# Kernel optimization log

Hardware: AMD Instinct MI355X
Metric: run time of the kernel (lower is better)

## Reference

```python
import jax, jax.numpy as jnp
import numpy as np

VOLRADIUS = 64.0
DT = 1.0 / VOLRADIUS          # normalized step size (dt / volradius)
NSTEPS = 64                   # covers t in [0, 1.0) at step DT


def setup_inputs() -> dict:
    key = jax.random.key(0)
    ks = jax.random.split(key, 8)
    B, H, W, K, M = 1, 128, 128, 32, 16
    # ray origins near volume center, unit directions
    raypos = 0.2 * jax.random.normal(ks[0], (B, H, W, 3), jnp.float32)
    rd = jax.random.normal(ks[1], (B, H, W, 3), jnp.float32)
    raydir = rd / jnp.linalg.norm(rd, axis=-1, keepdims=True)
    tmin = jnp.zeros((B, H, W), jnp.float32)
    tmax = 0.9 + 0.1 * jax.random.uniform(ks[2], (B, H, W), dtype=jnp.float32)
    tminmax = jnp.stack([tmin, tmax], axis=-1)
    # primitive poses: positions, rotations (orthonormal via QR), inverse-scales
    primpos = 0.3 * jax.random.normal(ks[3], (B, K, 3), jnp.float32)
    A = jax.random.normal(ks[4], (B, K, 3, 3), jnp.float32)
    primrot, _ = jnp.linalg.qr(A)
    primscale = 1.0 + 2.0 * jax.random.uniform(ks[5], (B, K, 3), dtype=jnp.float32)
    # RGBA voxel payload per primitive; alpha channel nonnegative (decoder emits nonneg density)
    template = jax.random.normal(ks[6], (B, K, 4, M, M, M), jnp.float32)
    template = template.at[:, :, 3].set(2.0 * jax.nn.softplus(template[:, :, 3]))
    return dict(raypos=raypos, raydir=raydir, tminmax=tminmax, primpos=primpos,
                primrot=primrot, primscale=primscale, template=template)


def _trilinear(template, y):
    # template [B,K,C,M,M,M]; y [B,R,K,3] normalized coords in [-1,1] (align_corners)
    B, K, C, M = template.shape[0], template.shape[1], template.shape[2], template.shape[3]
    g = (y + 1.0) * 0.5 * (M - 1)
    i0 = jnp.clip(jnp.floor(g), 0, M - 2).astype(jnp.int32)
    f = jnp.clip(g - i0.astype(g.dtype), 0.0, 1.0)
    i1 = i0 + 1
    bidx = jnp.arange(B)[:, None, None]
    kidx = jnp.arange(K)[None, None, :]

    def corner(iz, iy, ix):
        # advanced-index gather -> [B,R,K,C]
        return template[bidx, kidx, :, iz, iy, ix]

    fz, fy, fx = f[..., 0:1], f[..., 1:2], f[..., 2:3]
    i0z, i0y, i0x = i0[..., 0], i0[..., 1], i0[..., 2]
    i1z, i1y, i1x = i1[..., 0], i1[..., 1], i1[..., 2]
    v = ((1 - fz) * (1 - fy) * (1 - fx) * corner(i0z, i0y, i0x)
         + (1 - fz) * (1 - fy) * fx * corner(i0z, i0y, i1x)
         + (1 - fz) * fy * (1 - fx) * corner(i0z, i1y, i0x)
         + (1 - fz) * fy * fx * corner(i0z, i1y, i1x)
         + fz * (1 - fy) * (1 - fx) * corner(i1z, i0y, i0x)
         + fz * (1 - fy) * fx * corner(i1z, i0y, i1x)
         + fz * fy * (1 - fx) * corner(i1z, i1y, i0x)
         + fz * fy * fx * corner(i1z, i1y, i1x))
    return v  # [B,R,K,C]


def reference(raypos, raydir, tminmax, primpos, primrot, primscale, template):
    B, H, W, _ = raypos.shape
    R = H * W
    rp = raypos.reshape(B, R, 3)
    rd = raydir.reshape(B, R, 3)
    tmm = tminmax.reshape(B, R, 2)
    tmin, tmax = tmm[..., 0:1], tmm[..., 1:2]

    def step(carry, i):
        rgb, alpha = carry
        t = tmin + i * DT                                   # [B,R,1]
        pos = rp + rd * t                                   # [B,R,3]
        xl = pos[:, :, None, :] - primpos[:, None, :, :]    # [B,R,K,3]
        yloc = jnp.einsum('bkij,brkj->brki', primrot, xl) * primscale[:, None, :, :]
        inside = jnp.all(jnp.abs(yloc) <= 1.0, axis=-1, keepdims=True).astype(rgb.dtype)
        samp = (_trilinear(template, yloc) * inside).sum(axis=2)   # [B,R,4]
        srgb, salpha = samp[..., :3], samp[..., 3:4]
        valid = (t < tmax).astype(rgb.dtype)
        # clamped additive compositing (Neural Volumes / MVP)
        newalpha = jnp.clip(alpha + salpha * DT * valid, 0.0, 1.0)
        contrib = newalpha - alpha
        return (rgb + srgb * contrib, newalpha), None

    init = (jnp.zeros((B, R, 3), raypos.dtype), jnp.zeros((B, R, 1), raypos.dtype))
    (rgb, alpha), _ = jax.lax.scan(step, init, jnp.arange(NSTEPS, dtype=raypos.dtype))

    rayrgba = jnp.concatenate([rgb, alpha], axis=-1).reshape(B, H, W, 4)
    rayrgba = jnp.transpose(rayrgba, (0, 3, 1, 2))   # [B,4,H,W]
    rayrgb = rayrgba[:, :3]
    rayalpha = rayrgba[:, 3:4]
    return rayrgb, rayalpha, rayrgba
```

## Files before the change

### kernel.cpp

```cpp
#include <hip/hip_runtime.h>
#include <hip/hip_fp16.h>


namespace {

constexpr float kDT  = 1.0f / 64.0f;
constexpr int   kVox = 32 * 4096;

struct H4 { __half2 lo, hi; };
struct __attribute__((aligned(8))) H4x2 { __half2 l0, h0, l1, h1; };

__global__ __launch_bounds__(256) void transpose_tmpl_h(
    const float* __restrict__ tmpl, H4* __restrict__ wsH)
{
    const int idx = blockIdx.x * 256 + threadIdx.x;
    const int k   = idx >> 12;
    const int rem = idx & 4095;
    const float* src = tmpl + k * 16384 + rem;
    H4 v;
    v.lo = __floats2half2_rn(src[0],    src[4096]);
    v.hi = __floats2half2_rn(src[8192], src[12288]);
    wsH[idx] = v;
}

__device__ __forceinline__ __half2 lerp2(__half2 a, __half2 b, __half2 f) {
    return __hfma2(f, __hsub2(b, a), a);
}

template<int CTRL>
__device__ __forceinline__ float dpp_add(float v) {
    return v + __int_as_float(__builtin_amdgcn_update_dpp(
        0, __float_as_int(v), CTRL, 0xF, 0xF, true));
}

__device__ __forceinline__ float half_sum32(float v) {
    v = dpp_add<0xB1>(v);
    v = dpp_add<0x4E>(v);
    v = dpp_add<0x141>(v);
    v = dpp_add<0x140>(v);
    v += __int_as_float(__builtin_amdgcn_ds_swizzle(__float_as_int(v), 0x401F));
    return v;
}

__global__ __launch_bounds__(256) void raymarch12(
    const float* __restrict__ raypos,
    const float* __restrict__ raydir,
    const float* __restrict__ tminmax,
    const float* __restrict__ primpos,
    const float* __restrict__ primrot,
    const float* __restrict__ primscale,
    const H4* __restrict__ wsH,
    float* __restrict__ out,
    int R)
{
    const int lane   = threadIdx.x & 63;
    const int wid    = threadIdx.x >> 6;
    const int k      = lane & 31;
    const int parity = lane >> 5;
    const int ray    = blockIdx.x * 4 + wid;

    const float rpx = raypos[ray * 3 + 0];
    const float rpy = raypos[ray * 3 + 1];
    const float rpz = raypos[ray * 3 + 2];
    const float rdx = raydir[ray * 3 + 0];
    const float rdy = raydir[ray * 3 + 1];
    const float rdz = raydir[ray * 3 + 2];
    const float tmin = tminmax[ray * 2 + 0];
    const float tmax = tminmax[ray * 2 + 1];

    float A0, A1, A2, D0, D1, D2;
    {
        const float ox = rpx - primpos[k * 3 + 0];
        const float oy = rpy - primpos[k * 3 + 1];
        const float oz = rpz - primpos[k * 3 + 2];
        const float s0 = primscale[k * 3 + 0];
        const float s1 = primscale[k * 3 + 1];
        const float s2 = primscale[k * 3 + 2];
        const float* rk = primrot + k * 9;
        A0 = (rk[0] * ox + rk[1] * oy + rk[2] * oz) * s0;
        D0 = (rk[0] * rdx + rk[1] * rdy + rk[2] * rdz) * s0;
        A1 = (rk[3] * ox + rk[4] * oy + rk[5] * oz) * s1;
        D1 = (rk[3] * rdx + rk[4] * rdy + rk[5] * rdz) * s1;
        A2 = (rk[6] * ox + rk[7] * oy + rk[8] * oz) * s2;
        D2 = (rk[6] * rdx + rk[7] * rdy + rk[8] * rdz) * s2;
    }

    const H4* __restrict__ tbase = wsH + k * 4096;

    float alpha = 0.f;
    float r0 = 0.f, r1 = 0.f, r2 = 0.f;

    bool  inA, inB;
    int   adA, adB;
    float fzA, fyA, fxA, fzB, fyB, fxB;
    H4x2  a00, a01, a10, a11, b00, b01, b10, b11;

#define COORDS(J, IN, AD, FZ, FY, FX)                                    \
    {                                                                    \
        const float tl = fmaf((float)(2 * (J) + parity), kDT, tmin);     \
        const float y0 = fmaf(D0, tl, A0);                               \
        const float y1 = fmaf(D1, tl, A1);                               \
        const float y2 = fmaf(D2, tl, A2);                               \
        IN = ((J) < 32) && (tl < tmax) && fabsf(y0) <= 1.0f              \
           && fabsf(y1) <= 1.0f && fabsf(y2) <= 1.0f;                    \
        const float gz = fmaf(y0, 7.5f, 7.5f);                           \
        const float gy = fmaf(y1, 7.5f, 7.5f);                           \
        const float gx = fmaf(y2, 7.5f, 7.5f);                           \
        const int iz = min((int)gz, 14);                                 \
        const int iy = min((int)gy, 14);                                 \
        const int ix = min((int)gx, 14);                                 \
        FZ = fminf(gz - (float)iz, 1.0f);                                \
        FY = fminf(gy - (float)iy, 1.0f);                                \
        FX = fminf(gx - (float)ix, 1.0f);                                \
        AD = iz * 256 + iy * 16 + ix;                                    \
    }

#define PREF(IN, AD, P00, P01, P10, P11)                                 \
    if (IN) {                                                            \
        const H4* tp = tbase + (AD);                                     \
        P00 = *(const H4x2*)(tp + 0);                                    \
        P01 = *(const H4x2*)(tp + 16);                                   \
        P10 = *(const H4x2*)(tp + 256);                                  \
        P11 = *(const H4x2*)(tp + 272);                                  \
    }

#define CONSUME(J, IN, FZ, FY, FX, P00, P01, P10, P11)                   \
    {                                                                    \
        float s0 = 0.f, s1 = 0.f, s2 = 0.f, s3 = 0.f;                    \
        if (IN) {                                                        \
            const __half2 hz = __float2half2_rn(FZ);                     \
            const __half2 hy = __float2half2_rn(FY);                     \
            const __half2 hx = __float2half2_rn(FX);                     \
            const __half2 q0l0 = lerp2(P00.l0, P10.l0, hz);              \
            const __half2 q0h0 = lerp2(P00.h0, P10.h0, hz);              \
            const __half2 q0l1 = lerp2(P00.l1, P10.l1, hz);              \
            const __half2 q0h1 = lerp2(P00.h1, P10.h1, hz);              \
            const __half2 q1l0 = lerp2(P01.l0, P11.l0, hz);              \
            const __half2 q1h0 = lerp2(P01.h0, P11.h0, hz);              \
            const __half2 q1l1 = lerp2(P01.l1, P11.l1, hz);              \
            const __half2 q1h1 = lerp2(P01.h1, P11.h1, hz);              \
            const __half2 ul0 = lerp2(q0l0, q1l0, hy);                   \
            const __half2 uh0 = lerp2(q0h0, q1h0, hy);                   \
            const __half2 ul1 = lerp2(q0l1, q1l1, hy);                   \
            const __half2 uh1 = lerp2(q0h1, q1h1, hy);                   \
            const __half2 vl = lerp2(ul0, ul1, hx);                      \
            const __half2 vh = lerp2(uh0, uh1, hx);                      \
            const float2 fLo = __half22float2(vl);                       \
            const float2 fHi = __half22float2(vh);                       \
            s0 = fLo.x; s1 = fLo.y; s2 = fHi.x; s3 = fHi.y;              \
        }                                                                \
        if (__ballot(IN)) {                                              \
            float tot = half_sum32(s3);                                  \
            const float other = __shfl_xor(tot, 32);                     \
            const float te = parity ? other : tot;       \
            const float to = parity ? tot : other;       \
              \
            const float na1 = fminf(fmaf(te, kDT, alpha), 1.0f);         \
            const float c_e = na1 - alpha;                               \
            const float na2 = fminf(fmaf(to, kDT, na1), 1.0f);           \
            const float c_o = na2 - na1;                                 \
            alpha = na2;                                                 \
            const float contrib = parity ? c_o : c_e;                    \
            r0 = fmaf(s0, contrib, r0);                                  \
            r1 = fmaf(s1, contrib, r1);                                  \
            r2 = fmaf(s2, contrib, r2);                                  \
        }                                                                \
    }

    COORDS(0, inA, adA, fzA, fyA, fxA);
    PREF(inA, adA, a00, a01, a10, a11);

    for (int j = 0; ; ) {
        COORDS(j + 1, inB, adB, fzB, fyB, fxB);
        PREF(inB, adB, b00, b01, b10, b11);
        CONSUME(j, inA, fzA, fyA, fxA, a00, a01, a10, a11);
        ++j;
        {
            const float t0 = fmaf((float)(2 * j), kDT, tmin);
            if (j >= 32 || t0 >= tmax || alpha >= 1.0f) break;
        }
        COORDS(j + 1, inA, adA, fzA, fyA, fxA);
        PREF(inA, adA, a00, a01, a10, a11);
        CONSUME(j, inB, fzB, fyB, fxB, b00, b01, b10, b11);
        ++j;
        {
            const float t0 = fmaf((float)(2 * j), kDT, tmin);
            if (j >= 32 || t0 >= tmax || alpha >= 1.0f) break;
        }
    }

#undef COORDS
#undef PREF
#undef CONSUME

    r0 = half_sum32(r0); r0 += __shfl_xor(r0, 32);
    r1 = half_sum32(r1); r1 += __shfl_xor(r1, 32);
    r2 = half_sum32(r2); r2 += __shfl_xor(r2, 32);

    if (lane == 0) {
        out[0 * R + ray] = r0;
        out[1 * R + ray] = r1;
        out[2 * R + ray] = r2;
        out[3 * R + ray] = alpha;
        out[4 * R + ray] = r0;
        out[5 * R + ray] = r1;
        out[6 * R + ray] = r2;
        out[7 * R + ray] = alpha;
    }
}

__global__ __launch_bounds__(256) void raymarch_fb(
    const float* __restrict__ raypos, const float* __restrict__ raydir,
    const float* __restrict__ tminmax, const float* __restrict__ primpos,
    const float* __restrict__ primrot, const float* __restrict__ primscale,
    const float* __restrict__ tmpl, float* __restrict__ out, int R)
{
    const int lane = threadIdx.x & 63;
    const int wid  = threadIdx.x >> 6;
    const int k    = lane & 31;
    const int half = lane >> 5;
    const int ray  = blockIdx.x * 8 + wid * 2 + half;

    const float rpx = raypos[ray*3+0], rpy = raypos[ray*3+1], rpz = raypos[ray*3+2];
    const float rdx = raydir[ray*3+0], rdy = raydir[ray*3+1], rdz = raydir[ray*3+2];
    const float tmin = tminmax[ray*2+0], tmax = tminmax[ray*2+1];

    float A0,A1,A2,D0,D1,D2;
    {
        const float ox = rpx - primpos[k*3+0], oy = rpy - primpos[k*3+1], oz = rpz - primpos[k*3+2];
        const float s0 = primscale[k*3+0], s1 = primscale[k*3+1], s2 = primscale[k*3+2];
        const float* rk = primrot + k*9;
        A0 = (rk[0]*ox+rk[1]*oy+rk[2]*oz)*s0; D0 = (rk[0]*rdx+rk[1]*rdy+rk[2]*rdz)*s0;
        A1 = (rk[3]*ox+rk[4]*oy+rk[5]*oz)*s1; D1 = (rk[3]*rdx+rk[4]*rdy+rk[5]*rdz)*s1;
        A2 = (rk[6]*ox+rk[7]*oy+rk[8]*oz)*s2; D2 = (rk[6]*rdx+rk[7]*rdy+rk[8]*rdz)*s2;
    }
    float alpha = 0.f, r0 = 0.f, r1 = 0.f, r2 = 0.f;
    for (int i = 0; i < 64; ++i) {
        const float t = fmaf((float)i, kDT, tmin);
        const bool live = (t < tmax) && (alpha < 1.0f);
        if (__ballot(live) == 0ull) break;
        const float y0 = fmaf(D0,t,A0), y1 = fmaf(D1,t,A1), y2 = fmaf(D2,t,A2);
        const bool inside = live && fabsf(y0)<=1.f && fabsf(y1)<=1.f && fabsf(y2)<=1.f;
        if (__ballot(inside) == 0ull) continue;
        float s0=0.f,s1=0.f,s2=0.f,s3=0.f;
        if (inside) {
            const float gz=(y0+1.f)*7.5f, gy=(y1+1.f)*7.5f, gx=(y2+1.f)*7.5f;
            const int iz=(int)fminf(floorf(gz),14.f), iy=(int)fminf(floorf(gy),14.f), ix=(int)fminf(floorf(gx),14.f);
            const float fz=fminf(gz-(float)iz,1.f), fy=fminf(gy-(float)iy,1.f), fx=fminf(gx-(float)ix,1.f);
            const float oz_=1.f-fz, oy_=1.f-fy, ox_=1.f-fx;
            const float w000=oz_*oy_*ox_, w001=oz_*oy_*fx, w010=oz_*fy*ox_, w011=oz_*fy*fx;
            const float w100=fz*oy_*ox_, w101=fz*oy_*fx, w110=fz*fy*ox_, w111=fz*fy*fx;
            const float* tp = tmpl + k*16384 + iz*256 + iy*16 + ix;
            float acc[4];
            #pragma unroll
            for (int c = 0; c < 4; ++c) {
                const float* tc = tp + c*4096;
                acc[c] = w000*tc[0]+w001*tc[1]+w010*tc[16]+w011*tc[17]
                       + w100*tc[256]+w101*tc[257]+w110*tc[272]+w111*tc[273];
            }
            s0=acc[0]; s1=acc[1]; s2=acc[2]; s3=acc[3];
        }
        float tot3 = s3;
        #pragma unroll
        for (int m = 1; m < 32; m <<= 1) tot3 += __shfl_xor(tot3, m);
        const float na = fminf(fmaf(tot3, kDT, alpha), 1.0f);
        const float contrib = na - alpha;
        alpha = na;
        r0 = fmaf(s0, contrib, r0); r1 = fmaf(s1, contrib, r1); r2 = fmaf(s2, contrib, r2);
    }
    #pragma unroll
    for (int m = 1; m < 32; m <<= 1) {
        r0 += __shfl_xor(r0, m); r1 += __shfl_xor(r1, m); r2 += __shfl_xor(r2, m);
    }
    if (k == 0) {
        out[0*R+ray]=r0; out[1*R+ray]=r1; out[2*R+ray]=r2; out[3*R+ray]=alpha;
        out[4*R+ray]=r0; out[5*R+ray]=r1; out[6*R+ray]=r2; out[7*R+ray]=alpha;
    }
}

}

extern "C" void kernel_launch(void* const* d_in, const int* in_sizes, int n_in,
                              void* d_out, int out_size, void* d_ws, size_t ws_size,
                              hipStream_t stream) {
    const float* raypos    = (const float*)d_in[0];
    const float* raydir    = (const float*)d_in[1];
    const float* tminmax   = (const float*)d_in[2];
    const float* primpos   = (const float*)d_in[3];
    const float* primrot   = (const float*)d_in[4];
    const float* primscale = (const float*)d_in[5];
    const float* tmpl      = (const float*)d_in[6];
    float* out = (float*)d_out;

    const int R = in_sizes[0] / 3;
    const size_t needH = (size_t)kVox * sizeof(H4);

    if (ws_size >= needH) {
        H4* wsH = (H4*)d_ws;
        transpose_tmpl_h<<<dim3(kVox / 256), dim3(256), 0, stream>>>(tmpl, wsH);
        raymarch12<<<dim3(R / 4), dim3(256), 0, stream>>>(
            raypos, raydir, tminmax, primpos, primrot, primscale, wsH, out, R);
    } else {
        raymarch_fb<<<dim3(R / 8), dim3(256), 0, stream>>>(
            raypos, raydir, tminmax, primpos, primrot, primscale, tmpl, out, R);
    }
}
```

Baseline: 90.35 us.

## Process four steps per iteration instead of software-prefetched two-step pipeline

The explicit A/B prefetch double-buffering loop is replaced by a loop that handles four samples per iteration (two per lane parity), issuing both sets of gathers together and then running the compositing chain for all four. The aim is to halve loop and early-exit check overhead and the number of reductions per iteration, while still keeping two gathers in flight. The trade-off is that gathers are no longer issued an iteration ahead, so latency hiding depends on the compiler and on occupancy. Early termination is also coarser, so a ray may do up to one extra pair of samples after saturating.

```diff
diff --git a/kernel.cpp b/kernel.cpp
--- a/kernel.cpp
+++ b/kernel.cpp
@@ -42,7 +42,7 @@
     return v;
 }
 
-__global__ __launch_bounds__(256) void raymarch12(
+__global__ __launch_bounds__(256) void raymarch13(
     const float* __restrict__ raypos,
     const float* __restrict__ raydir,
     const float* __restrict__ tminmax,
@@ -90,18 +90,13 @@
     float alpha = 0.f;
     float r0 = 0.f, r1 = 0.f, r2 = 0.f;
 
-    bool  inA, inB;
-    int   adA, adB;
-    float fzA, fyA, fxA, fzB, fyB, fxB;
-    H4x2  a00, a01, a10, a11, b00, b01, b10, b11;
-
-#define COORDS(J, IN, AD, FZ, FY, FX)                                    \
+#define COORDS(SUB, IN, AD, FZ, FY, FX)                                  \
     {                                                                    \
-        const float tl = fmaf((float)(2 * (J) + parity), kDT, tmin);     \
+        const float tl = fmaf((float)(SUB), kDT, tmin);                  \
         const float y0 = fmaf(D0, tl, A0);                               \
         const float y1 = fmaf(D1, tl, A1);                               \
         const float y2 = fmaf(D2, tl, A2);                               \
-        IN = ((J) < 32) && (tl < tmax) && fabsf(y0) <= 1.0f              \
+        IN = (tl < tmax) && fabsf(y0) <= 1.0f                            \
            && fabsf(y1) <= 1.0f && fabsf(y2) <= 1.0f;                    \
         const float gz = fmaf(y0, 7.5f, 7.5f);                           \
         const float gy = fmaf(y1, 7.5f, 7.5f);                           \
@@ -115,30 +110,26 @@
         AD = iz * 256 + iy * 16 + ix;                                    \
     }
 
-#define PREF(IN, AD, P00, P01, P10, P11)                                 \
-    if (IN) {                                                            \
-        const H4* tp = tbase + (AD);                                     \
-        P00 = *(const H4x2*)(tp + 0);                                    \
-        P01 = *(const H4x2*)(tp + 16);                                   \
-        P10 = *(const H4x2*)(tp + 256);                                  \
-        P11 = *(const H4x2*)(tp + 272);                                  \
-    }
-
-#define CONSUME(J, IN, FZ, FY, FX, P00, P01, P10, P11)                   \
+#define EVAL(IN, AD, FZ, FY, FX, S0, S1, S2, S3)                         \
     {                                                                    \
-        float s0 = 0.f, s1 = 0.f, s2 = 0.f, s3 = 0.f;                    \
+        S0 = 0.f; S1 = 0.f; S2 = 0.f; S3 = 0.f;                         \
         if (IN) {                                                        \
+            const H4* tp = tbase + (AD);                                 \
+            const H4x2 p00 = *(const H4x2*)(tp + 0);                     \
+            const H4x2 p01 = *(const H4x2*)(tp + 16);                    \
+            const H4x2 p10 = *(const H4x2*)(tp + 256);                   \
+            const H4x2 p11 = *(const H4x2*)(tp + 272);                   \
             const __half2 hz = __float2half2_rn(FZ);                     \
             const __half2 hy = __float2half2_rn(FY);                     \
             const __half2 hx = __float2half2_rn(FX);                     \
-            const __half2 q0l0 = lerp2(P00.l0, P10.l0, hz);              \
-            const __half2 q0h0 = lerp2(P00.h0, P10.h0, hz);              \
-            const __half2 q0l1 = lerp2(P00.l1, P10.l1, hz);              \
-            const __half2 q0h1 = lerp2(P00.h1, P10.h1, hz);              \
-            const __half2 q1l0 = lerp2(P01.l0, P11.l0, hz);              \
-            const __half2 q1h0 = lerp2(P01.h0, P11.h0, hz);              \
-            const __half2 q1l1 = lerp2(P01.l1, P11.l1, hz);              \
-            const __half2 q1h1 = lerp2(P01.h1, P11.h1, hz);              \
+            const __half2 q0l0 = lerp2(p00.l0, p10.l0, hz);              \
+            const __half2 q0h0 = lerp2(p00.h0, p10.h0, hz);              \
+            const __half2 q0l1 = lerp2(p00.l1, p10.l1, hz);              \
+            const __half2 q0h1 = lerp2(p00.h1, p10.h1, hz);              \
+            const __half2 q1l0 = lerp2(p01.l0, p11.l0, hz);              \
+            const __half2 q1h0 = lerp2(p01.h0, p11.h0, hz);              \
+            const __half2 q1l1 = lerp2(p01.l1, p11.l1, hz);              \
+            const __half2 q1h1 = lerp2(p01.h1, p11.h1, hz);              \
             const __half2 ul0 = lerp2(q0l0, q1l0, hy);                   \
             const __half2 uh0 = lerp2(q0h0, q1h0, hy);                   \
             const __half2 ul1 = lerp2(q0l1, q1l1, hy);                   \
@@ -147,51 +138,54 @@
             const __half2 vh = lerp2(uh0, uh1, hx);                      \
             const float2 fLo = __half22float2(vl);                       \
             const float2 fHi = __half22float2(vh);                       \
-            s0 = fLo.x; s1 = fLo.y; s2 = fHi.x; s3 = fHi.y;              \
+            S0 = fLo.x; S1 = fLo.y; S2 = fHi.x; S3 = fHi.y;              \
         }                                                                \
-        if (__ballot(IN)) {                                              \
-            float tot = half_sum32(s3);                                  \
-            const float other = __shfl_xor(tot, 32);                     \
-            const float te = parity ? other : tot;       \
-            const float to = parity ? tot : other;       \
-              \
-            const float na1 = fminf(fmaf(te, kDT, alpha), 1.0f);         \
-            const float c_e = na1 - alpha;                               \
-            const float na2 = fminf(fmaf(to, kDT, na1), 1.0f);           \
-            const float c_o = na2 - na1;                                 \
-            alpha = na2;                                                 \
-            const float contrib = parity ? c_o : c_e;                    \
-            r0 = fmaf(s0, contrib, r0);                                  \
-            r1 = fmaf(s1, contrib, r1);                                  \
-            r2 = fmaf(s2, contrib, r2);                                  \
-        }                                                                \
-    }
-
-    COORDS(0, inA, adA, fzA, fyA, fxA);
-    PREF(inA, adA, a00, a01, a10, a11);
-
-    for (int j = 0; ; ) {
-        COORDS(j + 1, inB, adB, fzB, fyB, fxB);
-        PREF(inB, adB, b00, b01, b10, b11);
-        CONSUME(j, inA, fzA, fyA, fxA, a00, a01, a10, a11);
-        ++j;
-        {
-            const float t0 = fmaf((float)(2 * j), kDT, tmin);
-            if (j >= 32 || t0 >= tmax || alpha >= 1.0f) break;
+    }
+
+    for (int j = 0; j < 16; ++j) {
+        bool  inA, inB;
+        int   adA, adB;
+        float fzA, fyA, fxA, fzB, fyB, fxB;
+        COORDS(4 * j + parity,     inA, adA, fzA, fyA, fxA);
+        COORDS(4 * j + 2 + parity, inB, adB, fzB, fyB, fxB);
+
+        if (__ballot(inA || inB)) {
+            float s0a, s1a, s2a, s3a, s0b, s1b, s2b, s3b;
+            EVAL(inA, adA, fzA, fyA, fxA, s0a, s1a, s2a, s3a);
+            EVAL(inB, adB, fzB, fyB, fxB, s0b, s1b, s2b, s3b);
+
+            float ta = half_sum32(s3a);
+            float tb = half_sum32(s3b);
+            const float oa = __shfl_xor(ta, 32);
+            const float ob = __shfl_xor(tb, 32);
+            const float te0 = parity ? oa : ta;
+            const float to0 = parity ? ta : oa;
+            const float te1 = parity ? ob : tb;
+            const float to1 = parity ? tb : ob;
+
+            const float a1 = fminf(fmaf(te0, kDT, alpha), 1.0f);
+            const float c0 = a1 - alpha;
+            const float a2 = fminf(fmaf(to0, kDT, a1), 1.0f);
+            const float c1 = a2 - a1;
+            const float a3 = fminf(fmaf(te1, kDT, a2), 1.0f);
+            const float c2 = a3 - a2;
+            const float a4 = fminf(fmaf(to1, kDT, a3), 1.0f);
+            const float c3 = a4 - a3;
+            alpha = a4;
+
+            const float ca = parity ? c1 : c0;
+            const float cb = parity ? c3 : c2;
+            r0 = fmaf(s0a, ca, fmaf(s0b, cb, r0));
+            r1 = fmaf(s1a, ca, fmaf(s1b, cb, r1));
+            r2 = fmaf(s2a, ca, fmaf(s2b, cb, r2));
         }
-        COORDS(j + 1, inA, adA, fzA, fyA, fxA);
-        PREF(inA, adA, a00, a01, a10, a11);
-        CONSUME(j, inB, fzB, fyB, fxB, b00, b01, b10, b11);
-        ++j;
-        {
-            const float t0 = fmaf((float)(2 * j), kDT, tmin);
-            if (j >= 32 || t0 >= tmax || alpha >= 1.0f) break;
-        }
+
+        const float tn = fmaf((float)(4 * j + 4), kDT, tmin);
+        if (tn >= tmax || alpha >= 1.0f) break;
     }
 
 #undef COORDS
-#undef PREF
-#undef CONSUME
+#undef EVAL
 
     r0 = half_sum32(r0); r0 += __shfl_xor(r0, 32);
     r1 = half_sum32(r1); r1 += __shfl_xor(r1, 32);
@@ -298,7 +292,7 @@
     if (ws_size >= needH) {
         H4* wsH = (H4*)d_ws;
         transpose_tmpl_h<<<dim3(kVox / 256), dim3(256), 0, stream>>>(tmpl, wsH);
-        raymarch12<<<dim3(R / 4), dim3(256), 0, stream>>>(
+        raymarch13<<<dim3(R / 4), dim3(256), 0, stream>>>(
             raypos, raydir, tminmax, primpos, primrot, primscale, wsH, out, R);
     } else {
         raymarch_fb<<<dim3(R / 8), dim3(256), 0, stream>>>(
```

Result: faster. 86.83 us (-3.9%).
